# Optimization experiments

Hardware: AMD Instinct MI355X
Metric: run time of the kernel (lower is better)

## Reference

```python
import jax, jax.numpy as jnp
import numpy as np

B, L, HS, WS = 4, 5, 32, 32
C = 256            # dim == heads * dim_head
M, D = 8, 32       # heads, dim_head
T, R = 2, 4        # num_types, num_relations
I = M * D          # inner_dim
EPS = 1e-5


def setup_inputs() -> dict:
    key = jax.random.key(0)
    ks = jax.random.split(key, 12)
    w = 0.02
    x = jax.random.normal(ks[0], (B, L, HS, WS, C), dtype=jnp.float32)
    mask = jnp.ones((B, HS, WS, L, L), dtype=jnp.int32)
    prior_encoding = jax.random.randint(ks[1], (B, L, HS, WS, 3), 0, T).astype(jnp.float32)
    return {
        "x": x,
        "mask": mask,
        "prior_encoding": prior_encoding,
        "ln_w": jnp.ones((C,), jnp.float32),
        "ln_b": jnp.zeros((C,), jnp.float32),
        "Wq": jax.random.normal(ks[2], (T, C, I), jnp.float32) * w,
        "bq": jnp.zeros((T, I), jnp.float32),
        "Wk": jax.random.normal(ks[3], (T, C, I), jnp.float32) * w,
        "bk": jnp.zeros((T, I), jnp.float32),
        "Wv": jax.random.normal(ks[4], (T, C, I), jnp.float32) * w,
        "bv": jnp.zeros((T, I), jnp.float32),
        "Wa": jax.random.normal(ks[5], (T, I, C), jnp.float32) * w,
        "ba": jnp.zeros((T, C), jnp.float32),
        "rel_att": jax.random.normal(ks[6], (R, M, D, D), jnp.float32) * w,
        "rel_msg": jax.random.normal(ks[7], (R, M, D, D), jnp.float32) * w,
    }


def _hgt_forward(x, mask, prior_encoding, ln_w, ln_b, Wq, bq, Wk, bk, Wv, bv, Wa, ba, rel_att, rel_msg):
    # pre-LayerNorm over channel dim
    mu = jnp.mean(x, axis=-1, keepdims=True)
    var = jnp.mean(jnp.square(x - mu), axis=-1, keepdims=True)
    xn = (x - mu) * jax.lax.rsqrt(var + EPS) * ln_w + ln_b

    # [B,L,H,W,C] -> [B,H,W,L,C]
    xp = jnp.transpose(xn, (0, 2, 3, 1, 4))
    types = prior_encoding[:, :, 0, 0, 2].astype(jnp.int32)  # [B,L]

    # per-type q/k/v projections via gather of type-indexed weights
    q = jnp.einsum('bhwlc,blci->bhwli', xp, Wq[types]) + bq[types][:, None, None]
    k = jnp.einsum('bhwlc,blci->bhwli', xp, Wk[types]) + bk[types][:, None, None]
    v = jnp.einsum('bhwlc,blci->bhwli', xp, Wv[types]) + bv[types][:, None, None]

    def to_heads(t):  # [B,H,W,L,I] -> [B,M,H,W,L,D]
        return jnp.transpose(t.reshape(B, HS, WS, L, M, D), (0, 4, 1, 2, 3, 5))
    q, k, v = to_heads(q), to_heads(k), to_heads(v)

    # relation-indexed edge weights: e_type = t_i * T + t_j
    e = types[:, :, None] * T + types[:, None, :]              # [B,L,L]
    w_att = jnp.transpose(rel_att[e], (0, 3, 1, 2, 4, 5))      # [B,M,L,L,D,D]
    w_msg = jnp.transpose(rel_msg[e], (0, 3, 1, 2, 4, 5))

    scale = D ** -0.5
    q_w = jnp.einsum('bmhwip,bmijpq->bmhwijq', q, w_att)
    att = jnp.einsum('bmhwijq,bmhwjq->bmhwij', q_w, k) * scale
    att = jnp.where(mask[:, None] == 0, -1e9, att)
    att = jax.nn.softmax(att, axis=-1)

    v_msg = jnp.einsum('bmijpc,bmhwjp->bmhwijc', w_msg, v)
    out = jnp.einsum('bmhwij,bmhwijc->bmhwic', att, v_msg)

    # [B,M,H,W,L,D] -> [B,H,W,L,C]
    out = jnp.transpose(out, (0, 2, 3, 4, 1, 5)).reshape(B, HS, WS, L, I)
    out = jnp.einsum('bhwli,blic->bhwlc', out, Wa[types]) + ba[types][:, None, None]
    # dropout is identity at inference
    return jnp.transpose(out, (0, 3, 1, 2, 4))                 # [B,L,H,W,C]


def reference(x, mask, prior_encoding, ln_w, ln_b, Wq, bq, Wk, bk, Wv, bv, Wa, ba, rel_att, rel_msg):
    return _hgt_forward(x, mask, prior_encoding, ln_w, ln_b, Wq, bq, Wk, bk, Wv, bv, Wa, ba, rel_att, rel_msg)
```

## Files before the change

### kernel.cpp

```cpp
#include <hip/hip_runtime.h>
#include <hip/hip_bf16.h>
#include <math.h>

#define BB 4
#define LL 5
#define HSZ 32
#define WSZ 32
#define PP (HSZ*WSZ)
#define CC 256
#define MM 8
#define DD 32
#define II 256
#define TT 2
#define NTOK (BB*PP*LL*II)
#define TILE_ELEMS 8192
#define SCALE 0.17677669529663687f

typedef short bf16x8 __attribute__((ext_vector_type(8)));
typedef float f32x4 __attribute__((ext_vector_type(4)));

static __device__ __forceinline__ ushort f2bf(float f) {
    unsigned u = __float_as_uint(f);
    unsigned r = (u + 0x7fffu + ((u >> 16) & 1u)) >> 16;
    return (ushort)r;
}
static __device__ __forceinline__ float bf2f(ushort u) {
    return __uint_as_float(((unsigned)u) << 16);
}

__global__ __launch_bounds__(256) void k_fold(
    const float* __restrict__ Wq, const float* __restrict__ Wv,
    const float* __restrict__ Wk, const float* __restrict__ Wa,
    const float* __restrict__ bq, const float* __restrict__ bv,
    const float* __restrict__ rel_att, const float* __restrict__ rel_msg,
    const float* __restrict__ x,
    const float* __restrict__ lnw, const float* __restrict__ lnb,
    ushort* __restrict__ packW, float* __restrict__ bEff,
    ushort* __restrict__ xnPack)
{
    __shared__ float As[1024];
    __shared__ ushort Apack[8192];
    const int blk = blockIdx.x;
    const int tid = threadIdx.x;

    if (blk < 64) {
        const int p  = blk >> 5;
        const int t  = (blk >> 4) & 1;
        const int ts = (blk >> 3) & 1;
        const int m  = blk & 7;
        const float* A = (p == 0)
            ? rel_att + (size_t)((t * 2 + ts) * 8 + m) * 1024
            : rel_msg + (size_t)((ts * 2 + t) * 8 + m) * 1024;
        for (int i = tid; i < 1024; i += 256) As[i] = A[i];
        __syncthreads();

        const float* W = ((p == 0) ? Wq : Wv) + (size_t)t * 65536;
        const int k = tid;
        float wrow[32];
        #pragma unroll
        for (int u = 0; u < 8; ++u)
            *(float4*)&wrow[u * 4] = *(const float4*)&W[k * 256 + m * 32 + u * 4];

        const int slot = (p == 0 ? 0 : 4) + t * 2 + ts;
        ushort* base = packW + (size_t)slot * 65536;
        const int kt = k >> 5, j = k & 7, lq = ((k >> 3) & 3) * 16;
        #pragma unroll
        for (int q = 0; q < 32; ++q) {
            float acc = 0.f;
            #pragma unroll
            for (int pp = 0; pp < 32; ++pp) acc += wrow[pp] * As[pp * 32 + q];
            const int nt = m * 2 + (q >> 4);
            const int lane = lq + (q & 15);
            base[(size_t)((nt * 8 + kt) * 64 + lane) * 8 + j] = f2bf(acc);
        }
        if (tid < 32) {
            const int q = tid;
            const float* bi = ((p == 0) ? bq : bv) + t * 256 + m * 32;
            float acc = 0.f;
            #pragma unroll
            for (int pp = 0; pp < 32; ++pp) acc += bi[pp] * As[pp * 32 + q];
            bEff[(p ? 1024 : 0) + (t * 2 + ts) * 256 + m * 32 + q] = acc;
        }
    } else if (blk < 192) {
        const int idx = blk - 64;
        const int which = idx >> 6;
        const int gi = (idx & 63) * 256 + tid;
        const int t = gi >> 13;
        const int sub = gi & 8191;
        const float* src = ((which == 0) ? Wk : Wa) + (size_t)t * 65536;
        const int slot = (which == 0 ? 8 : 10) + t;
        const int nt = sub >> 9, kt = (sub >> 6) & 7, lane = sub & 63;
        const int k0 = kt * 32 + (lane >> 4) * 8;
        const int n  = nt * 16 + (lane & 15);
        ushort h[8];
        #pragma unroll
        for (int j = 0; j < 8; ++j) h[j] = f2bf(src[(size_t)(k0 + j) * 256 + n]);
        uint4 o;
        o.x = (unsigned)h[0] | ((unsigned)h[1] << 16);
        o.y = (unsigned)h[2] | ((unsigned)h[3] << 16);
        o.z = (unsigned)h[4] | ((unsigned)h[5] << 16);
        o.w = (unsigned)h[6] | ((unsigned)h[7] << 16);
        *(uint4*)(packW + (size_t)slot * 65536 + (size_t)sub * 8) = o;
    } else {
        const int lblk = blk - 192;
        const int bl  = lblk >> 5;
        const int pt  = lblk & 31;
        const int p0  = pt * 32;

        const int r  = tid >> 3;
        const int jj = tid & 7;
        const float* xrow = x + ((size_t)bl * PP + p0 + r) * CC;
        float4 xv[8];
        float s1 = 0.f, s2 = 0.f;
        #pragma unroll
        for (int u = 0; u < 8; ++u) {
            xv[u] = *(const float4*)(xrow + jj * 32 + u * 4);
            s1 += xv[u].x + xv[u].y + xv[u].z + xv[u].w;
            s2 += xv[u].x * xv[u].x + xv[u].y * xv[u].y + xv[u].z * xv[u].z + xv[u].w * xv[u].w;
        }
        s1 += __shfl_xor(s1, 1); s1 += __shfl_xor(s1, 2); s1 += __shfl_xor(s1, 4);
        s2 += __shfl_xor(s2, 1); s2 += __shfl_xor(s2, 2); s2 += __shfl_xor(s2, 4);
        const float mu   = s1 * (1.0f / 256.0f);
        const float var  = s2 * (1.0f / 256.0f) - mu * mu;
        const float rstd = rsqrtf(var + 1e-5f);

        const int mt_r = r >> 4, rm = r & 15;
        #pragma unroll
        for (int u = 0; u < 8; ++u) {
            const int c0 = jj * 32 + u * 4;
            const float4 g  = *(const float4*)(lnw + c0);
            const float4 bt = *(const float4*)(lnb + c0);
            const ushort h0 = f2bf((xv[u].x - mu) * rstd * g.x + bt.x);
            const ushort h1 = f2bf((xv[u].y - mu) * rstd * g.y + bt.y);
            const ushort h2 = f2bf((xv[u].z - mu) * rstd * g.z + bt.z);
            const ushort h3 = f2bf((xv[u].w - mu) * rstd * g.w + bt.w);
            uint2 w2;
            w2.x = (unsigned)h0 | ((unsigned)h1 << 16);
            w2.y = (unsigned)h2 | ((unsigned)h3 << 16);
            const int kt   = c0 >> 5;
            const int lsub = rm + (((c0 >> 3) & 3) << 4);
            const int j0   = c0 & 7;
            *(uint2*)&Apack[(((mt_r * 8 + kt) * 64 + lsub) << 3) + j0] = w2;
        }
        __syncthreads();

        const size_t tbase = (size_t)lblk * TILE_ELEMS;
        #pragma unroll
        for (int u = 0; u < 4; ++u) {
            const int ch = (tid + u * 256) * 8;
            *(uint4*)&xnPack[tbase + ch] = *(const uint4*)&Apack[ch];
        }
    }
}

__global__ __launch_bounds__(256) void k_proj(
    const ushort* __restrict__ xnPack, const float* __restrict__ prior,
    const ushort* __restrict__ packW, const float* __restrict__ bEff,
    const float* __restrict__ bk,
    ushort* __restrict__ qw0, ushort* __restrict__ qw1, ushort* __restrict__ kkO,
    ushort* __restrict__ vm0, ushort* __restrict__ vm1)
{
    __shared__ ushort As[8192];

    const int tid  = threadIdx.x;
    const int blk  = blockIdx.x;
    const int mat  = blk / 640;
    const int rem  = blk - mat * 640;
    const int bl   = rem >> 5;
    const int sub  = rem & 31;
    const int pg   = sub >> 1;
    const int half = sub & 1;
    const int t    = (int)prior[(size_t)bl * (PP * 3) + 2];

    int slot; const float* bias;
    if (mat < 2)       { slot = t * 2 + mat;           bias = bEff + slot * 256; }
    else if (mat == 2) { slot = 8 + t;                 bias = bk + t * 256; }
    else               { slot = 4 + t * 2 + (mat - 3); bias = bEff + 1024 + (t * 2 + (mat - 3)) * 256; }
    ushort* dst = (mat == 0) ? qw0 : (mat == 1) ? qw1 : (mat == 2) ? kkO : (mat == 3) ? vm0 : vm1;

    const int wv = tid >> 6, lane = tid & 63;

    const ushort* Bp = packW + (size_t)slot * 65536;
    bf16x8 bfr[8][2];
    #pragma unroll
    for (int kt = 0; kt < 8; ++kt)
        #pragma unroll
        for (int nn = 0; nn < 2; ++nn) {
            const int ntg = half * 8 + wv * 2 + nn;
            bfr[kt][nn] = *(const bf16x8*)&Bp[(size_t)((ntg * 8 + kt) * 64 + lane) * 8];
        }

    const int cl = lane & 15, rq = lane >> 4;
    const int colA = half * 128 + wv * 32 + cl;
    const int colB = colA + 16;
    const float biasA = bias[colA], biasB = bias[colB];

    #pragma unroll 1
    for (int tl = 0; tl < 2; ++tl) {
        const int pt = pg * 2 + tl;
        const size_t tbase = (size_t)(bl * 32 + pt) * TILE_ELEMS;
        __syncthreads();
        #pragma unroll
        for (int u = 0; u < 4; ++u) {
            const int ch = (tid + u * 256) * 8;
            *(uint4*)&As[ch] = *(const uint4*)&xnPack[tbase + ch];
        }
        __syncthreads();

        f32x4 acc[2][2];
        #pragma unroll
        for (int mt = 0; mt < 2; ++mt)
            #pragma unroll
            for (int nn = 0; nn < 2; ++nn)
                acc[mt][nn] = (f32x4){0.f, 0.f, 0.f, 0.f};

        #pragma unroll
        for (int kt = 0; kt < 8; ++kt) {
            const bf16x8 a0 = *(const bf16x8*)&As[((0 * 8 + kt) * 64 + lane) << 3];
            const bf16x8 a1 = *(const bf16x8*)&As[((1 * 8 + kt) * 64 + lane) << 3];
            acc[0][0] = __builtin_amdgcn_mfma_f32_16x16x32_bf16(a0, bfr[kt][0], acc[0][0], 0, 0, 0);
            acc[0][1] = __builtin_amdgcn_mfma_f32_16x16x32_bf16(a0, bfr[kt][1], acc[0][1], 0, 0, 0);
            acc[1][0] = __builtin_amdgcn_mfma_f32_16x16x32_bf16(a1, bfr[kt][0], acc[1][0], 0, 0, 0);
            acc[1][1] = __builtin_amdgcn_mfma_f32_16x16x32_bf16(a1, bfr[kt][1], acc[1][1], 0, 0, 0);
        }

        const int p0 = pt * 32;
        #pragma unroll
        for (int mt = 0; mt < 2; ++mt) {
            const int row0 = p0 + mt * 16 + rq * 4;
            #pragma unroll
            for (int r2 = 0; r2 < 4; ++r2) {
                const size_t rb = ((size_t)bl * PP + row0 + r2) * II;
                dst[rb + colA] = f2bf(acc[mt][0][r2] + biasA);
                dst[rb + colB] = f2bf(acc[mt][1][r2] + biasB);
            }
        }
    }
}

__global__ __launch_bounds__(256) void k_attn(
    const ushort* __restrict__ qw0, const ushort* __restrict__ qw1,
    const ushort* __restrict__ kkI,
    const ushort* __restrict__ vm0, const ushort* __restrict__ vm1,
    const int* __restrict__ mask, const float* __restrict__ prior,
    ushort* __restrict__ ao)
{
    const int tid  = threadIdx.x;
    const int site = blockIdx.x * 4 + (tid >> 6);
    const int lane = tid & 63;
    const int b    = site >> 10;
    const int pix  = site & 1023;
    const int c0   = lane * 4;

    const int usite = __builtin_amdgcn_readfirstlane(site);
    const int ub    = usite >> 10;

    int ty[5];
    #pragma unroll
    for (int l = 0; l < 5; ++l)
        ty[l] = (int)prior[(size_t)(ub * 5 + l) * (PP * 3) + 2];

    int mv[5][5];
    #pragma unroll
    for (int i = 0; i < 5; ++i)
        #pragma unroll
        for (int j = 0; j < 5; ++j)
            mv[i][j] = mask[(size_t)usite * 25 + i * 5 + j];

    float qf[2][5][4], kf[5][4];
    #pragma unroll
    for (int l = 0; l < 5; ++l) {
        const size_t base = (((size_t)(b * 5 + l) << 10) + pix) * II + c0;
        const ushort4 q0 = *(const ushort4*)(qw0 + base);
        const ushort4 q1 = *(const ushort4*)(qw1 + base);
        const ushort4 kv = *(const ushort4*)(kkI + base);
        qf[0][l][0] = bf2f(q0.x); qf[0][l][1] = bf2f(q0.y); qf[0][l][2] = bf2f(q0.z); qf[0][l][3] = bf2f(q0.w);
        qf[1][l][0] = bf2f(q1.x); qf[1][l][1] = bf2f(q1.y); qf[1][l][2] = bf2f(q1.z); qf[1][l][3] = bf2f(q1.w);
        kf[l][0]    = bf2f(kv.x); kf[l][1]    = bf2f(kv.y); kf[l][2]    = bf2f(kv.z); kf[l][3]    = bf2f(kv.w);
    }

    float s[5][5];
    #pragma unroll
    for (int j = 0; j < 5; ++j) {
        if (ty[j]) {
            #pragma unroll
            for (int i = 0; i < 5; ++i)
                s[i][j] = qf[1][i][0] * kf[j][0] + qf[1][i][1] * kf[j][1]
                        + qf[1][i][2] * kf[j][2] + qf[1][i][3] * kf[j][3];
        } else {
            #pragma unroll
            for (int i = 0; i < 5; ++i)
                s[i][j] = qf[0][i][0] * kf[j][0] + qf[0][i][1] * kf[j][1]
                        + qf[0][i][2] * kf[j][2] + qf[0][i][3] * kf[j][3];
        }
    }
    #pragma unroll
    for (int i = 0; i < 5; ++i)
        #pragma unroll
        for (int j = 0; j < 5; ++j) s[i][j] += __shfl_xor(s[i][j], 1);
    #pragma unroll
    for (int i = 0; i < 5; ++i)
        #pragma unroll
        for (int j = 0; j < 5; ++j) s[i][j] += __shfl_xor(s[i][j], 2);
    #pragma unroll
    for (int i = 0; i < 5; ++i)
        #pragma unroll
        for (int j = 0; j < 5; ++j) s[i][j] += __shfl_xor(s[i][j], 4);

    float vf[2][5][4];
    #pragma unroll
    for (int l = 0; l < 5; ++l) {
        const size_t base = (((size_t)(b * 5 + l) << 10) + pix) * II + c0;
        const ushort4 v0 = *(const ushort4*)(vm0 + base);
        const ushort4 v1 = *(const ushort4*)(vm1 + base);
        vf[0][l][0] = bf2f(v0.x); vf[0][l][1] = bf2f(v0.y); vf[0][l][2] = bf2f(v0.z); vf[0][l][3] = bf2f(v0.w);
        vf[1][l][0] = bf2f(v1.x); vf[1][l][1] = bf2f(v1.y); vf[1][l][2] = bf2f(v1.z); vf[1][l][3] = bf2f(v1.w);
    }

    #pragma unroll
    for (int i = 0; i < 5; ++i) {
        float lg[5];
        #pragma unroll
        for (int j = 0; j < 5; ++j)
            lg[j] = mv[i][j] ? s[i][j] * SCALE : -1e9f;
        const float mx = fmaxf(fmaxf(fmaxf(lg[0], lg[1]), fmaxf(lg[2], lg[3])), lg[4]);
        float ex[5], sum = 0.f;
        #pragma unroll
        for (int j = 0; j < 5; ++j) { ex[j] = __expf(lg[j] - mx); sum += ex[j]; }
        const float rs = 1.0f / sum;
        float o0 = 0.f, o1 = 0.f, o2 = 0.f, o3 = 0.f;
        if (ty[i]) {
            #pragma unroll
            for (int j = 0; j < 5; ++j) {
                o0 += ex[j] * vf[1][j][0]; o1 += ex[j] * vf[1][j][1];
                o2 += ex[j] * vf[1][j][2]; o3 += ex[j] * vf[1][j][3];
            }
        } else {
            #pragma unroll
            for (int j = 0; j < 5; ++j) {
                o0 += ex[j] * vf[0][j][0]; o1 += ex[j] * vf[0][j][1];
                o2 += ex[j] * vf[0][j][2]; o3 += ex[j] * vf[0][j][3];
            }
        }
        o0 *= rs; o1 *= rs; o2 *= rs; o3 *= rs;
        uint2 w2;
        w2.x = (unsigned)f2bf(o0) | ((unsigned)f2bf(o1) << 16);
        w2.y = (unsigned)f2bf(o2) | ((unsigned)f2bf(o3) << 16);
        *(uint2*)&ao[(((size_t)(b * 5 + i) << 10) + pix) * II + c0] = w2;
    }
}

__global__ __launch_bounds__(256) void k_out(
    const ushort* __restrict__ ao, const float* __restrict__ prior,
    const ushort* __restrict__ packW, const float* __restrict__ ba,
    float* __restrict__ out)
{
    __shared__ float obufF[32 * 132];

    const int tid  = threadIdx.x;
    const int blk  = blockIdx.x;
    const int bl   = blk >> 6;
    const int sub  = blk & 63;
    const int pt   = sub >> 1;
    const int half = sub & 1;
    const int bbi  = bl / LL;
    const int l    = bl - bbi * LL;
    const int t    = (int)prior[(size_t)bl * (PP * 3) + 2];

    const int wv = tid >> 6, lane = tid & 63;
    const ushort* Bp = packW + (size_t)(10 + t) * 65536;
    bf16x8 bfr[8][2];
    #pragma unroll
    for (int kt = 0; kt < 8; ++kt)
        #pragma unroll
        for (int nn = 0; nn < 2; ++nn) {
            const int ntg = half * 8 + wv * 2 + nn;
            bfr[kt][nn] = *(const bf16x8*)&Bp[(size_t)((ntg * 8 + kt) * 64 + lane) * 8];
        }

    const int p0   = pt * 32;
    const int rowA = lane & 15;
    const int ksub = (lane >> 4) * 8;
    const ushort* a_base = ao + ((size_t)(bl * PP + p0 + rowA)) * II + ksub;

    const int cl = lane & 15, rq = lane >> 4;
    const int colL_A = wv * 32 + cl;
    const int colL_B = colL_A + 16;
    const float biasA = ba[t * CC + half * 128 + colL_A];
    const float biasB = ba[t * CC + half * 128 + colL_B];

    f32x4 acc[2][2];
    #pragma unroll
    for (int mt = 0; mt < 2; ++mt)
        #pragma unroll
        for (int nn = 0; nn < 2; ++nn)
            acc[mt][nn] = (f32x4){0.f, 0.f, 0.f, 0.f};

    #pragma unroll
    for (int kt = 0; kt < 8; ++kt) {
        const bf16x8 a0 = *(const bf16x8*)(a_base + kt * 32);
        const bf16x8 a1 = *(const bf16x8*)(a_base + (size_t)16 * II + kt * 32);
        acc[0][0] = __builtin_amdgcn_mfma_f32_16x16x32_bf16(a0, bfr[kt][0], acc[0][0], 0, 0, 0);
        acc[0][1] = __builtin_amdgcn_mfma_f32_16x16x32_bf16(a0, bfr[kt][1], acc[0][1], 0, 0, 0);
        acc[1][0] = __builtin_amdgcn_mfma_f32_16x16x32_bf16(a1, bfr[kt][0], acc[1][0], 0, 0, 0);
        acc[1][1] = __builtin_amdgcn_mfma_f32_16x16x32_bf16(a1, bfr[kt][1], acc[1][1], 0, 0, 0);
    }

    #pragma unroll
    for (int mt = 0; mt < 2; ++mt) {
        const int rowb = mt * 16 + rq * 4;
        #pragma unroll
        for (int r2 = 0; r2 < 4; ++r2) {
            obufF[(rowb + r2) * 132 + colL_A] = acc[mt][0][r2] + biasA;
            obufF[(rowb + r2) * 132 + colL_B] = acc[mt][1][r2] + biasB;
        }
    }
    __syncthreads();

    #pragma unroll
    for (int k2 = 0; k2 < 4; ++k2) {
        const int id  = tid + k2 * 256;
        const int row = id >> 5;
        const int ch  = (id & 31) * 4;
        const float4 v4 = *(const float4*)&obufF[row * 132 + ch];
        *(float4*)(out + ((size_t)(bbi * LL + l) * PP + p0 + row) * CC + half * 128 + ch) = v4;
    }
}

extern "C" void kernel_launch(void* const* d_in, const int* in_sizes, int n_in,
                              void* d_out, int out_size, void* d_ws, size_t ws_size,
                              hipStream_t stream) {
    const float* x       = (const float*)d_in[0];
    const int*   mask    = (const int*)d_in[1];
    const float* prior   = (const float*)d_in[2];
    const float* lnw     = (const float*)d_in[3];
    const float* lnb     = (const float*)d_in[4];
    const float* Wq      = (const float*)d_in[5];
    const float* bq      = (const float*)d_in[6];
    const float* Wk      = (const float*)d_in[7];
    const float* bk      = (const float*)d_in[8];
    const float* Wv      = (const float*)d_in[9];
    const float* bv      = (const float*)d_in[10];
    const float* Wa      = (const float*)d_in[11];
    const float* ba      = (const float*)d_in[12];
    const float* rel_att = (const float*)d_in[13];
    const float* rel_msg = (const float*)d_in[14];
    float* out = (float*)d_out;

    ushort* qw0    = (ushort*)d_ws;
    ushort* qw1    = qw0 + NTOK;
    ushort* kko    = qw1 + NTOK;
    ushort* vm0    = kko + NTOK;
    ushort* vm1    = vm0 + NTOK;
    ushort* ao     = vm1 + NTOK;
    ushort* xnPack = ao + NTOK;
    ushort* packW  = xnPack + NTOK;
    float*  bEff   = (float*)(packW + 12 * 65536);

    hipLaunchKernelGGL(k_fold, dim3(832), dim3(256), 0, stream,
                       Wq, Wv, Wk, Wa, bq, bv, rel_att, rel_msg,
                       x, lnw, lnb, packW, bEff, xnPack);
    hipLaunchKernelGGL(k_proj, dim3(3200), dim3(256), 0, stream,
                       xnPack, prior, packW, bEff, bk, qw0, qw1, kko, vm0, vm1);
    hipLaunchKernelGGL(k_attn, dim3(1024), dim3(256), 0, stream,
                       qw0, qw1, kko, vm0, vm1, mask, prior, ao);
    hipLaunchKernelGGL(k_out, dim3(1280), dim3(256), 0, stream,
                       ao, prior, packW, ba, out);
}
```

Baseline: 154.9 us.

## Fuse four stage kernels into one persistent cooperative kernel with grid syncs

Replaces the four separate launches (fold/LayerNorm, projection, attention, output projection) with one cooperative persistent kernel. Blocks grid-stride over the work of each stage, and grid.sync separates the stages. The projection stage now processes one tile per work unit and reloads the B fragments each time, where before each block handled two tiles. This removes the gaps between launches and the launch overhead. In exchange it adds grid-wide barriers, caps occupancy through launch bounds, and makes every stage share one register and LDS budget.

```diff
diff --git a/kernel.cpp b/kernel.cpp
--- a/kernel.cpp
+++ b/kernel.cpp
@@ -1,6 +1,9 @@
 #include <hip/hip_runtime.h>
+#include <hip/hip_cooperative_groups.h>
 #include <hip/hip_bf16.h>
 #include <math.h>
+
+namespace cg = cooperative_groups;
 
 #define BB 4
 #define LL 5
@@ -28,183 +31,180 @@
     return __uint_as_float(((unsigned)u) << 16);
 }
 
-__global__ __launch_bounds__(256) void k_fold(
-    const float* __restrict__ Wq, const float* __restrict__ Wv,
-    const float* __restrict__ Wk, const float* __restrict__ Wa,
-    const float* __restrict__ bq, const float* __restrict__ bv,
-    const float* __restrict__ rel_att, const float* __restrict__ rel_msg,
-    const float* __restrict__ x,
-    const float* __restrict__ lnw, const float* __restrict__ lnb,
-    ushort* __restrict__ packW, float* __restrict__ bEff,
-    ushort* __restrict__ xnPack)
+struct MegaArgs {
+    const float* x; const int* mask; const float* prior;
+    const float* lnw; const float* lnb;
+    const float* Wq; const float* bq; const float* Wk; const float* bk;
+    const float* Wv; const float* bv; const float* Wa; const float* ba;
+    const float* rel_att; const float* rel_msg;
+    ushort* qw0; ushort* qw1; ushort* kko; ushort* vm0; ushort* vm1;
+    ushort* ao; ushort* xnPack; ushort* packW; float* bEff;
+    float* out;
+};
+
+union SMem {
+    struct { float As[1024]; ushort Apack[8192]; } f;
+    ushort As16[8192];
+    float  obufF[32 * 132];
+};
+
+__global__ __launch_bounds__(256, 4) void k_mega(MegaArgs g)
 {
-    __shared__ float As[1024];
-    __shared__ ushort Apack[8192];
-    const int blk = blockIdx.x;
+    __shared__ SMem sm;
+    cg::grid_group grid = cg::this_grid();
+
     const int tid = threadIdx.x;
-
-    if (blk < 64) {
-        const int p  = blk >> 5;
-        const int t  = (blk >> 4) & 1;
-        const int ts = (blk >> 3) & 1;
-        const int m  = blk & 7;
-        const float* A = (p == 0)
-            ? rel_att + (size_t)((t * 2 + ts) * 8 + m) * 1024
-            : rel_msg + (size_t)((ts * 2 + t) * 8 + m) * 1024;
-        for (int i = tid; i < 1024; i += 256) As[i] = A[i];
+    const int bid = blockIdx.x;
+    const int NB  = gridDim.x;
+    const int wv = tid >> 6, lane = tid & 63;
+
+    for (int blk = bid; blk < 832; blk += NB) {
         __syncthreads();
-
-        const float* W = ((p == 0) ? Wq : Wv) + (size_t)t * 65536;
-        const int k = tid;
-        float wrow[32];
-        #pragma unroll
-        for (int u = 0; u < 8; ++u)
-            *(float4*)&wrow[u * 4] = *(const float4*)&W[k * 256 + m * 32 + u * 4];
-
-        const int slot = (p == 0 ? 0 : 4) + t * 2 + ts;
-        ushort* base = packW + (size_t)slot * 65536;
-        const int kt = k >> 5, j = k & 7, lq = ((k >> 3) & 3) * 16;
-        #pragma unroll
-        for (int q = 0; q < 32; ++q) {
-            float acc = 0.f;
-            #pragma unroll
-            for (int pp = 0; pp < 32; ++pp) acc += wrow[pp] * As[pp * 32 + q];
-            const int nt = m * 2 + (q >> 4);
-            const int lane = lq + (q & 15);
-            base[(size_t)((nt * 8 + kt) * 64 + lane) * 8 + j] = f2bf(acc);
-        }
-        if (tid < 32) {
-            const int q = tid;
-            const float* bi = ((p == 0) ? bq : bv) + t * 256 + m * 32;
-            float acc = 0.f;
-            #pragma unroll
-            for (int pp = 0; pp < 32; ++pp) acc += bi[pp] * As[pp * 32 + q];
-            bEff[(p ? 1024 : 0) + (t * 2 + ts) * 256 + m * 32 + q] = acc;
-        }
-    } else if (blk < 192) {
-        const int idx = blk - 64;
-        const int which = idx >> 6;
-        const int gi = (idx & 63) * 256 + tid;
-        const int t = gi >> 13;
-        const int sub = gi & 8191;
-        const float* src = ((which == 0) ? Wk : Wa) + (size_t)t * 65536;
-        const int slot = (which == 0 ? 8 : 10) + t;
-        const int nt = sub >> 9, kt = (sub >> 6) & 7, lane = sub & 63;
-        const int k0 = kt * 32 + (lane >> 4) * 8;
-        const int n  = nt * 16 + (lane & 15);
-        ushort h[8];
-        #pragma unroll
-        for (int j = 0; j < 8; ++j) h[j] = f2bf(src[(size_t)(k0 + j) * 256 + n]);
-        uint4 o;
-        o.x = (unsigned)h[0] | ((unsigned)h[1] << 16);
-        o.y = (unsigned)h[2] | ((unsigned)h[3] << 16);
-        o.z = (unsigned)h[4] | ((unsigned)h[5] << 16);
-        o.w = (unsigned)h[6] | ((unsigned)h[7] << 16);
-        *(uint4*)(packW + (size_t)slot * 65536 + (size_t)sub * 8) = o;
-    } else {
-        const int lblk = blk - 192;
-        const int bl  = lblk >> 5;
-        const int pt  = lblk & 31;
-        const int p0  = pt * 32;
-
-        const int r  = tid >> 3;
-        const int jj = tid & 7;
-        const float* xrow = x + ((size_t)bl * PP + p0 + r) * CC;
-        float4 xv[8];
-        float s1 = 0.f, s2 = 0.f;
-        #pragma unroll
-        for (int u = 0; u < 8; ++u) {
-            xv[u] = *(const float4*)(xrow + jj * 32 + u * 4);
-            s1 += xv[u].x + xv[u].y + xv[u].z + xv[u].w;
-            s2 += xv[u].x * xv[u].x + xv[u].y * xv[u].y + xv[u].z * xv[u].z + xv[u].w * xv[u].w;
-        }
-        s1 += __shfl_xor(s1, 1); s1 += __shfl_xor(s1, 2); s1 += __shfl_xor(s1, 4);
-        s2 += __shfl_xor(s2, 1); s2 += __shfl_xor(s2, 2); s2 += __shfl_xor(s2, 4);
-        const float mu   = s1 * (1.0f / 256.0f);
-        const float var  = s2 * (1.0f / 256.0f) - mu * mu;
-        const float rstd = rsqrtf(var + 1e-5f);
-
-        const int mt_r = r >> 4, rm = r & 15;
-        #pragma unroll
-        for (int u = 0; u < 8; ++u) {
-            const int c0 = jj * 32 + u * 4;
-            const float4 g  = *(const float4*)(lnw + c0);
-            const float4 bt = *(const float4*)(lnb + c0);
-            const ushort h0 = f2bf((xv[u].x - mu) * rstd * g.x + bt.x);
-            const ushort h1 = f2bf((xv[u].y - mu) * rstd * g.y + bt.y);
-            const ushort h2 = f2bf((xv[u].z - mu) * rstd * g.z + bt.z);
-            const ushort h3 = f2bf((xv[u].w - mu) * rstd * g.w + bt.w);
-            uint2 w2;
-            w2.x = (unsigned)h0 | ((unsigned)h1 << 16);
-            w2.y = (unsigned)h2 | ((unsigned)h3 << 16);
-            const int kt   = c0 >> 5;
-            const int lsub = rm + (((c0 >> 3) & 3) << 4);
-            const int j0   = c0 & 7;
-            *(uint2*)&Apack[(((mt_r * 8 + kt) * 64 + lsub) << 3) + j0] = w2;
-        }
+        if (blk < 64) {
+            const int p  = blk >> 5;
+            const int t  = (blk >> 4) & 1;
+            const int ts = (blk >> 3) & 1;
+            const int m  = blk & 7;
+            const float* A = (p == 0)
+                ? g.rel_att + (size_t)((t * 2 + ts) * 8 + m) * 1024
+                : g.rel_msg + (size_t)((ts * 2 + t) * 8 + m) * 1024;
+            for (int i = tid; i < 1024; i += 256) sm.f.As[i] = A[i];
+            __syncthreads();
+
+            const float* W = ((p == 0) ? g.Wq : g.Wv) + (size_t)t * 65536;
+            const int k = tid;
+            float wrow[32];
+            #pragma unroll
+            for (int u = 0; u < 8; ++u)
+                *(float4*)&wrow[u * 4] = *(const float4*)&W[k * 256 + m * 32 + u * 4];
+
+            const int slot = (p == 0 ? 0 : 4) + t * 2 + ts;
+            ushort* base = g.packW + (size_t)slot * 65536;
+            const int kt = k >> 5, j = k & 7, lq = ((k >> 3) & 3) * 16;
+            #pragma unroll
+            for (int q = 0; q < 32; ++q) {
+                float acc = 0.f;
+                #pragma unroll
+                for (int pp = 0; pp < 32; ++pp) acc += wrow[pp] * sm.f.As[pp * 32 + q];
+                const int nt = m * 2 + (q >> 4);
+                const int ln2 = lq + (q & 15);
+                base[(size_t)((nt * 8 + kt) * 64 + ln2) * 8 + j] = f2bf(acc);
+            }
+            if (tid < 32) {
+                const int q = tid;
+                const float* bi = ((p == 0) ? g.bq : g.bv) + t * 256 + m * 32;
+                float acc = 0.f;
+                #pragma unroll
+                for (int pp = 0; pp < 32; ++pp) acc += bi[pp] * sm.f.As[pp * 32 + q];
+                g.bEff[(p ? 1024 : 0) + (t * 2 + ts) * 256 + m * 32 + q] = acc;
+            }
+        } else if (blk < 192) {
+            const int idx = blk - 64;
+            const int which = idx >> 6;
+            const int gi = (idx & 63) * 256 + tid;
+            const int t = gi >> 13;
+            const int sub = gi & 8191;
+            const float* src = ((which == 0) ? g.Wk : g.Wa) + (size_t)t * 65536;
+            const int slot = (which == 0 ? 8 : 10) + t;
+            const int nt = sub >> 9, kt = (sub >> 6) & 7, ln2 = sub & 63;
+            const int k0 = kt * 32 + (ln2 >> 4) * 8;
+            const int n  = nt * 16 + (ln2 & 15);
+            ushort h[8];
+            #pragma unroll
+            for (int j = 0; j < 8; ++j) h[j] = f2bf(src[(size_t)(k0 + j) * 256 + n]);
+            uint4 o;
+            o.x = (unsigned)h[0] | ((unsigned)h[1] << 16);
+            o.y = (unsigned)h[2] | ((unsigned)h[3] << 16);
+            o.z = (unsigned)h[4] | ((unsigned)h[5] << 16);
+            o.w = (unsigned)h[6] | ((unsigned)h[7] << 16);
+            *(uint4*)(g.packW + (size_t)slot * 65536 + (size_t)sub * 8) = o;
+        } else {
+            const int lblk = blk - 192;
+            const int bl  = lblk >> 5;
+            const int pt  = lblk & 31;
+            const int p0  = pt * 32;
+
+            const int r  = tid >> 3;
+            const int jj = tid & 7;
+            const float* xrow = g.x + ((size_t)bl * PP + p0 + r) * CC;
+            float4 xv[8];
+            float s1 = 0.f, s2 = 0.f;
+            #pragma unroll
+            for (int u = 0; u < 8; ++u) {
+                xv[u] = *(const float4*)(xrow + jj * 32 + u * 4);
+                s1 += xv[u].x + xv[u].y + xv[u].z + xv[u].w;
+                s2 += xv[u].x * xv[u].x + xv[u].y * xv[u].y + xv[u].z * xv[u].z + xv[u].w * xv[u].w;
+            }
+            s1 += __shfl_xor(s1, 1); s1 += __shfl_xor(s1, 2); s1 += __shfl_xor(s1, 4);
+            s2 += __shfl_xor(s2, 1); s2 += __shfl_xor(s2, 2); s2 += __shfl_xor(s2, 4);
+            const float mu   = s1 * (1.0f / 256.0f);
+            const float var  = s2 * (1.0f / 256.0f) - mu * mu;
+            const float rstd = rsqrtf(var + 1e-5f);
+
+            const int mt_r = r >> 4, rm = r & 15;
+            #pragma unroll
+            for (int u = 0; u < 8; ++u) {
+                const int c0 = jj * 32 + u * 4;
+                const float4 gg = *(const float4*)(g.lnw + c0);
+                const float4 bt = *(const float4*)(g.lnb + c0);
+                const ushort h0 = f2bf((xv[u].x - mu) * rstd * gg.x + bt.x);
+                const ushort h1 = f2bf((xv[u].y - mu) * rstd * gg.y + bt.y);
+                const ushort h2 = f2bf((xv[u].z - mu) * rstd * gg.z + bt.z);
+                const ushort h3 = f2bf((xv[u].w - mu) * rstd * gg.w + bt.w);
+                uint2 w2;
+                w2.x = (unsigned)h0 | ((unsigned)h1 << 16);
+                w2.y = (unsigned)h2 | ((unsigned)h3 << 16);
+                const int kt   = c0 >> 5;
+                const int lsub = rm + (((c0 >> 3) & 3) << 4);
+                const int j0   = c0 & 7;
+                *(uint2*)&sm.f.Apack[(((mt_r * 8 + kt) * 64 + lsub) << 3) + j0] = w2;
+            }
+            __syncthreads();
+
+            const size_t tbase = (size_t)lblk * TILE_ELEMS;
+            #pragma unroll
+            for (int u = 0; u < 4; ++u) {
+                const int ch = (tid + u * 256) * 8;
+                *(uint4*)&g.xnPack[tbase + ch] = *(const uint4*)&sm.f.Apack[ch];
+            }
+        }
+    }
+
+    __threadfence();
+    grid.sync();
+
+    for (int u = bid; u < 6400; u += NB) {
+        const int mat  = u / 1280;
+        const int rem  = u - mat * 1280;
+        const int bl   = rem >> 6;
+        const int sub  = rem & 63;
+        const int pt   = sub >> 1;
+        const int half = sub & 1;
+        const int t    = (int)g.prior[(size_t)bl * (PP * 3) + 2];
+
+        int slot; const float* bias;
+        if (mat < 2)       { slot = t * 2 + mat;           bias = g.bEff + slot * 256; }
+        else if (mat == 2) { slot = 8 + t;                 bias = g.bk + t * 256; }
+        else               { slot = 4 + t * 2 + (mat - 3); bias = g.bEff + 1024 + (t * 2 + (mat - 3)) * 256; }
+        ushort* dst = (mat == 0) ? g.qw0 : (mat == 1) ? g.qw1 : (mat == 2) ? g.kko : (mat == 3) ? g.vm0 : g.vm1;
+
         __syncthreads();
-
-        const size_t tbase = (size_t)lblk * TILE_ELEMS;
-        #pragma unroll
-        for (int u = 0; u < 4; ++u) {
-            const int ch = (tid + u * 256) * 8;
-            *(uint4*)&xnPack[tbase + ch] = *(const uint4*)&Apack[ch];
-        }
-    }
-}
-
-__global__ __launch_bounds__(256) void k_proj(
-    const ushort* __restrict__ xnPack, const float* __restrict__ prior,
-    const ushort* __restrict__ packW, const float* __restrict__ bEff,
-    const float* __restrict__ bk,
-    ushort* __restrict__ qw0, ushort* __restrict__ qw1, ushort* __restrict__ kkO,
-    ushort* __restrict__ vm0, ushort* __restrict__ vm1)
-{
-    __shared__ ushort As[8192];
-
-    const int tid  = threadIdx.x;
-    const int blk  = blockIdx.x;
-    const int mat  = blk / 640;
-    const int rem  = blk - mat * 640;
-    const int bl   = rem >> 5;
-    const int sub  = rem & 31;
-    const int pg   = sub >> 1;
-    const int half = sub & 1;
-    const int t    = (int)prior[(size_t)bl * (PP * 3) + 2];
-
-    int slot; const float* bias;
-    if (mat < 2)       { slot = t * 2 + mat;           bias = bEff + slot * 256; }
-    else if (mat == 2) { slot = 8 + t;                 bias = bk + t * 256; }
-    else               { slot = 4 + t * 2 + (mat - 3); bias = bEff + 1024 + (t * 2 + (mat - 3)) * 256; }
-    ushort* dst = (mat == 0) ? qw0 : (mat == 1) ? qw1 : (mat == 2) ? kkO : (mat == 3) ? vm0 : vm1;
-
-    const int wv = tid >> 6, lane = tid & 63;
-
-    const ushort* Bp = packW + (size_t)slot * 65536;
-    bf16x8 bfr[8][2];
-    #pragma unroll
-    for (int kt = 0; kt < 8; ++kt)
-        #pragma unroll
-        for (int nn = 0; nn < 2; ++nn) {
-            const int ntg = half * 8 + wv * 2 + nn;
-            bfr[kt][nn] = *(const bf16x8*)&Bp[(size_t)((ntg * 8 + kt) * 64 + lane) * 8];
-        }
-
-    const int cl = lane & 15, rq = lane >> 4;
-    const int colA = half * 128 + wv * 32 + cl;
-    const int colB = colA + 16;
-    const float biasA = bias[colA], biasB = bias[colB];
-
-    #pragma unroll 1
-    for (int tl = 0; tl < 2; ++tl) {
-        const int pt = pg * 2 + tl;
         const size_t tbase = (size_t)(bl * 32 + pt) * TILE_ELEMS;
-        __syncthreads();
-        #pragma unroll
-        for (int u = 0; u < 4; ++u) {
-            const int ch = (tid + u * 256) * 8;
-            *(uint4*)&As[ch] = *(const uint4*)&xnPack[tbase + ch];
-        }
+        #pragma unroll
+        for (int uu = 0; uu < 4; ++uu) {
+            const int ch = (tid + uu * 256) * 8;
+            *(uint4*)&sm.As16[ch] = *(const uint4*)&g.xnPack[tbase + ch];
+        }
+
+        const ushort* Bp = g.packW + (size_t)slot * 65536;
+        bf16x8 bfr[8][2];
+        #pragma unroll
+        for (int kt = 0; kt < 8; ++kt)
+            #pragma unroll
+            for (int nn = 0; nn < 2; ++nn) {
+                const int ntg = half * 8 + wv * 2 + nn;
+                bfr[kt][nn] = *(const bf16x8*)&Bp[(size_t)((ntg * 8 + kt) * 64 + lane) * 8];
+            }
         __syncthreads();
 
         f32x4 acc[2][2];
@@ -216,14 +216,18 @@
 
         #pragma unroll
         for (int kt = 0; kt < 8; ++kt) {
-            const bf16x8 a0 = *(const bf16x8*)&As[((0 * 8 + kt) * 64 + lane) << 3];
-            const bf16x8 a1 = *(const bf16x8*)&As[((1 * 8 + kt) * 64 + lane) << 3];
+            const bf16x8 a0 = *(const bf16x8*)&sm.As16[((0 * 8 + kt) * 64 + lane) << 3];
+            const bf16x8 a1 = *(const bf16x8*)&sm.As16[((1 * 8 + kt) * 64 + lane) << 3];
             acc[0][0] = __builtin_amdgcn_mfma_f32_16x16x32_bf16(a0, bfr[kt][0], acc[0][0], 0, 0, 0);
             acc[0][1] = __builtin_amdgcn_mfma_f32_16x16x32_bf16(a0, bfr[kt][1], acc[0][1], 0, 0, 0);
             acc[1][0] = __builtin_amdgcn_mfma_f32_16x16x32_bf16(a1, bfr[kt][0], acc[1][0], 0, 0, 0);
             acc[1][1] = __builtin_amdgcn_mfma_f32_16x16x32_bf16(a1, bfr[kt][1], acc[1][1], 0, 0, 0);
         }
 
+        const int cl = lane & 15, rq = lane >> 4;
+        const int colA = half * 128 + wv * 32 + cl;
+        const int colB = colA + 16;
+        const float biasA = bias[colA], biasB = bias[colB];
         const int p0 = pt * 32;
         #pragma unroll
         for (int mt = 0; mt < 2; ++mt) {
@@ -236,234 +240,230 @@
             }
         }
     }
-}
-
-__global__ __launch_bounds__(256) void k_attn(
-    const ushort* __restrict__ qw0, const ushort* __restrict__ qw1,
-    const ushort* __restrict__ kkI,
-    const ushort* __restrict__ vm0, const ushort* __restrict__ vm1,
-    const int* __restrict__ mask, const float* __restrict__ prior,
-    ushort* __restrict__ ao)
-{
-    const int tid  = threadIdx.x;
-    const int site = blockIdx.x * 4 + (tid >> 6);
-    const int lane = tid & 63;
-    const int b    = site >> 10;
-    const int pix  = site & 1023;
-    const int c0   = lane * 4;
-
-    const int usite = __builtin_amdgcn_readfirstlane(site);
-    const int ub    = usite >> 10;
-
-    int ty[5];
-    #pragma unroll
-    for (int l = 0; l < 5; ++l)
-        ty[l] = (int)prior[(size_t)(ub * 5 + l) * (PP * 3) + 2];
-
-    int mv[5][5];
-    #pragma unroll
-    for (int i = 0; i < 5; ++i)
-        #pragma unroll
-        for (int j = 0; j < 5; ++j)
-            mv[i][j] = mask[(size_t)usite * 25 + i * 5 + j];
-
-    float qf[2][5][4], kf[5][4];
-    #pragma unroll
-    for (int l = 0; l < 5; ++l) {
-        const size_t base = (((size_t)(b * 5 + l) << 10) + pix) * II + c0;
-        const ushort4 q0 = *(const ushort4*)(qw0 + base);
-        const ushort4 q1 = *(const ushort4*)(qw1 + base);
-        const ushort4 kv = *(const ushort4*)(kkI + base);
-        qf[0][l][0] = bf2f(q0.x); qf[0][l][1] = bf2f(q0.y); qf[0][l][2] = bf2f(q0.z); qf[0][l][3] = bf2f(q0.w);
-        qf[1][l][0] = bf2f(q1.x); qf[1][l][1] = bf2f(q1.y); qf[1][l][2] = bf2f(q1.z); qf[1][l][3] = bf2f(q1.w);
-        kf[l][0]    = bf2f(kv.x); kf[l][1]    = bf2f(kv.y); kf[l][2]    = bf2f(kv.z); kf[l][3]    = bf2f(kv.w);
+
+    __threadfence();
+    grid.sync();
+
+    for (int u = bid; u < 1024; u += NB) {
+        const int site = u * 4 + (tid >> 6);
+        const int b    = site >> 10;
+        const int pix  = site & 1023;
+        const int c0   = lane * 4;
+
+        const int usite = __builtin_amdgcn_readfirstlane(site);
+        const int ub    = usite >> 10;
+
+        int ty[5];
+        #pragma unroll
+        for (int l = 0; l < 5; ++l)
+            ty[l] = (int)g.prior[(size_t)(ub * 5 + l) * (PP * 3) + 2];
+
+        int mv[5][5];
+        #pragma unroll
+        for (int i = 0; i < 5; ++i)
+            #pragma unroll
+            for (int j = 0; j < 5; ++j)
+                mv[i][j] = g.mask[(size_t)usite * 25 + i * 5 + j];
+
+        float qf[2][5][4], kf[5][4];
+        #pragma unroll
+        for (int l = 0; l < 5; ++l) {
+            const size_t base = (((size_t)(b * 5 + l) << 10) + pix) * II + c0;
+            const ushort4 q0 = *(const ushort4*)(g.qw0 + base);
+            const ushort4 q1 = *(const ushort4*)(g.qw1 + base);
+            const ushort4 kv = *(const ushort4*)(g.kko + base);
+            qf[0][l][0] = bf2f(q0.x); qf[0][l][1] = bf2f(q0.y); qf[0][l][2] = bf2f(q0.z); qf[0][l][3] = bf2f(q0.w);
+            qf[1][l][0] = bf2f(q1.x); qf[1][l][1] = bf2f(q1.y); qf[1][l][2] = bf2f(q1.z); qf[1][l][3] = bf2f(q1.w);
+            kf[l][0]    = bf2f(kv.x); kf[l][1]    = bf2f(kv.y); kf[l][2]    = bf2f(kv.z); kf[l][3]    = bf2f(kv.w);
+        }
+
+        float s[5][5];
+        #pragma unroll
+        for (int j = 0; j < 5; ++j) {
+            if (ty[j]) {
+                #pragma unroll
+                for (int i = 0; i < 5; ++i)
+                    s[i][j] = qf[1][i][0] * kf[j][0] + qf[1][i][1] * kf[j][1]
+                            + qf[1][i][2] * kf[j][2] + qf[1][i][3] * kf[j][3];
+            } else {
+                #pragma unroll
+                for (int i = 0; i < 5; ++i)
+                    s[i][j] = qf[0][i][0] * kf[j][0] + qf[0][i][1] * kf[j][1]
+                            + qf[0][i][2] * kf[j][2] + qf[0][i][3] * kf[j][3];
+            }
+        }
+        #pragma unroll
+        for (int i = 0; i < 5; ++i)
+            #pragma unroll
+            for (int j = 0; j < 5; ++j) s[i][j] += __shfl_xor(s[i][j], 1);
+        #pragma unroll
+        for (int i = 0; i < 5; ++i)
+            #pragma unroll
+            for (int j = 0; j < 5; ++j) s[i][j] += __shfl_xor(s[i][j], 2);
+        #pragma unroll
+        for (int i = 0; i < 5; ++i)
+            #pragma unroll
+            for (int j = 0; j < 5; ++j) s[i][j] += __shfl_xor(s[i][j], 4);
+
+        float vf[2][5][4];
+        #pragma unroll
+        for (int l = 0; l < 5; ++l) {
+            const size_t base = (((size_t)(b * 5 + l) << 10) + pix) * II + c0;
+            const ushort4 v0 = *(const ushort4*)(g.vm0 + base);
+            const ushort4 v1 = *(const ushort4*)(g.vm1 + base);
+            vf[0][l][0] = bf2f(v0.x); vf[0][l][1] = bf2f(v0.y); vf[0][l][2] = bf2f(v0.z); vf[0][l][3] = bf2f(v0.w);
+            vf[1][l][0] = bf2f(v1.x); vf[1][l][1] = bf2f(v1.y); vf[1][l][2] = bf2f(v1.z); vf[1][l][3] = bf2f(v1.w);
+        }
+
+        #pragma unroll
+        for (int i = 0; i < 5; ++i) {
+            float lg[5];
+            #pragma unroll
+            for (int j = 0; j < 5; ++j)
+                lg[j] = mv[i][j] ? s[i][j] * SCALE : -1e9f;
+            const float mx = fmaxf(fmaxf(fmaxf(lg[0], lg[1]), fmaxf(lg[2], lg[3])), lg[4]);
+            float ex[5], sum = 0.f;
+            #pragma unroll
+            for (int j = 0; j < 5; ++j) { ex[j] = __expf(lg[j] - mx); sum += ex[j]; }
+            const float rs = 1.0f / sum;
+            float o0 = 0.f, o1 = 0.f, o2 = 0.f, o3 = 0.f;
+            if (ty[i]) {
+                #pragma unroll
+                for (int j = 0; j < 5; ++j) {
+                    o0 += ex[j] * vf[1][j][0]; o1 += ex[j] * vf[1][j][1];
+                    o2 += ex[j] * vf[1][j][2]; o3 += ex[j] * vf[1][j][3];
+                }
+            } else {
+                #pragma unroll
+                for (int j = 0; j < 5; ++j) {
+                    o0 += ex[j] * vf[0][j][0]; o1 += ex[j] * vf[0][j][1];
+                    o2 += ex[j] * vf[0][j][2]; o3 += ex[j] * vf[0][j][3];
+                }
+            }
+            o0 *= rs; o1 *= rs; o2 *= rs; o3 *= rs;
+            uint2 w2;
+            w2.x = (unsigned)f2bf(o0) | ((unsigned)f2bf(o1) << 16);
+            w2.y = (unsigned)f2bf(o2) | ((unsigned)f2bf(o3) << 16);
+            *(uint2*)&g.ao[(((size_t)(b * 5 + i) << 10) + pix) * II + c0] = w2;
+        }
     }
 
-    float s[5][5];
-    #pragma unroll
-    for (int j = 0; j < 5; ++j) {
-        if (ty[j]) {
-            #pragma unroll
-            for (int i = 0; i < 5; ++i)
-                s[i][j] = qf[1][i][0] * kf[j][0] + qf[1][i][1] * kf[j][1]
-                        + qf[1][i][2] * kf[j][2] + qf[1][i][3] * kf[j][3];
-        } else {
-            #pragma unroll
-            for (int i = 0; i < 5; ++i)
-                s[i][j] = qf[0][i][0] * kf[j][0] + qf[0][i][1] * kf[j][1]
-                        + qf[0][i][2] * kf[j][2] + qf[0][i][3] * kf[j][3];
-        }
-    }
-    #pragma unroll
-    for (int i = 0; i < 5; ++i)
-        #pragma unroll
-        for (int j = 0; j < 5; ++j) s[i][j] += __shfl_xor(s[i][j], 1);
-    #pragma unroll
-    for (int i = 0; i < 5; ++i)
-        #pragma unroll
-        for (int j = 0; j < 5; ++j) s[i][j] += __shfl_xor(s[i][j], 2);
-    #pragma unroll
-    for (int i = 0; i < 5; ++i)
-        #pragma unroll
-        for (int j = 0; j < 5; ++j) s[i][j] += __shfl_xor(s[i][j], 4);
-
-    float vf[2][5][4];
-    #pragma unroll
-    for (int l = 0; l < 5; ++l) {
-        const size_t base = (((size_t)(b * 5 + l) << 10) + pix) * II + c0;
-        const ushort4 v0 = *(const ushort4*)(vm0 + base);
-        const ushort4 v1 = *(const ushort4*)(vm1 + base);
-        vf[0][l][0] = bf2f(v0.x); vf[0][l][1] = bf2f(v0.y); vf[0][l][2] = bf2f(v0.z); vf[0][l][3] = bf2f(v0.w);
-        vf[1][l][0] = bf2f(v1.x); vf[1][l][1] = bf2f(v1.y); vf[1][l][2] = bf2f(v1.z); vf[1][l][3] = bf2f(v1.w);
-    }
-
-    #pragma unroll
-    for (int i = 0; i < 5; ++i) {
-        float lg[5];
-        #pragma unroll
-        for (int j = 0; j < 5; ++j)
-            lg[j] = mv[i][j] ? s[i][j] * SCALE : -1e9f;
-        const float mx = fmaxf(fmaxf(fmaxf(lg[0], lg[1]), fmaxf(lg[2], lg[3])), lg[4]);
-        float ex[5], sum = 0.f;
-        #pragma unroll
-        for (int j = 0; j < 5; ++j) { ex[j] = __expf(lg[j] - mx); sum += ex[j]; }
-        const float rs = 1.0f / sum;
-        float o0 = 0.f, o1 = 0.f, o2 = 0.f, o3 = 0.f;
-        if (ty[i]) {
-            #pragma unroll
-            for (int j = 0; j < 5; ++j) {
-                o0 += ex[j] * vf[1][j][0]; o1 += ex[j] * vf[1][j][1];
-                o2 += ex[j] * vf[1][j][2]; o3 += ex[j] * vf[1][j][3];
-            }
-        } else {
-            #pragma unroll
-            for (int j = 0; j < 5; ++j) {
-                o0 += ex[j] * vf[0][j][0]; o1 += ex[j] * vf[0][j][1];
-                o2 += ex[j] * vf[0][j][2]; o3 += ex[j] * vf[0][j][3];
-            }
-        }
-        o0 *= rs; o1 *= rs; o2 *= rs; o3 *= rs;
-        uint2 w2;
-        w2.x = (unsigned)f2bf(o0) | ((unsigned)f2bf(o1) << 16);
-        w2.y = (unsigned)f2bf(o2) | ((unsigned)f2bf(o3) << 16);
-        *(uint2*)&ao[(((size_t)(b * 5 + i) << 10) + pix) * II + c0] = w2;
-    }
-}
-
-__global__ __launch_bounds__(256) void k_out(
-    const ushort* __restrict__ ao, const float* __restrict__ prior,
-    const ushort* __restrict__ packW, const float* __restrict__ ba,
-    float* __restrict__ out)
-{
-    __shared__ float obufF[32 * 132];
-
-    const int tid  = threadIdx.x;
-    const int blk  = blockIdx.x;
-    const int bl   = blk >> 6;
-    const int sub  = blk & 63;
-    const int pt   = sub >> 1;
-    const int half = sub & 1;
-    const int bbi  = bl / LL;
-    const int l    = bl - bbi * LL;
-    const int t    = (int)prior[(size_t)bl * (PP * 3) + 2];
-
-    const int wv = tid >> 6, lane = tid & 63;
-    const ushort* Bp = packW + (size_t)(10 + t) * 65536;
-    bf16x8 bfr[8][2];
-    #pragma unroll
-    for (int kt = 0; kt < 8; ++kt)
-        #pragma unroll
-        for (int nn = 0; nn < 2; ++nn) {
-            const int ntg = half * 8 + wv * 2 + nn;
-            bfr[kt][nn] = *(const bf16x8*)&Bp[(size_t)((ntg * 8 + kt) * 64 + lane) * 8];
-        }
-
-    const int p0   = pt * 32;
-    const int rowA = lane & 15;
-    const int ksub = (lane >> 4) * 8;
-    const ushort* a_base = ao + ((size_t)(bl * PP + p0 + rowA)) * II + ksub;
-
-    const int cl = lane & 15, rq = lane >> 4;
-    const int colL_A = wv * 32 + cl;
-    const int colL_B = colL_A + 16;
-    const float biasA = ba[t * CC + half * 128 + colL_A];
-    const float biasB = ba[t * CC + half * 128 + colL_B];
-
-    f32x4 acc[2][2];
-    #pragma unroll
-    for (int mt = 0; mt < 2; ++mt)
-        #pragma unroll
-        for (int nn = 0; nn < 2; ++nn)
-            acc[mt][nn] = (f32x4){0.f, 0.f, 0.f, 0.f};
-
-    #pragma unroll
-    for (int kt = 0; kt < 8; ++kt) {
-        const bf16x8 a0 = *(const bf16x8*)(a_base + kt * 32);
-        const bf16x8 a1 = *(const bf16x8*)(a_base + (size_t)16 * II + kt * 32);
-        acc[0][0] = __builtin_amdgcn_mfma_f32_16x16x32_bf16(a0, bfr[kt][0], acc[0][0], 0, 0, 0);
-        acc[0][1] = __builtin_amdgcn_mfma_f32_16x16x32_bf16(a0, bfr[kt][1], acc[0][1], 0, 0, 0);
-        acc[1][0] = __builtin_amdgcn_mfma_f32_16x16x32_bf16(a1, bfr[kt][0], acc[1][0], 0, 0, 0);
-        acc[1][1] = __builtin_amdgcn_mfma_f32_16x16x32_bf16(a1, bfr[kt][1], acc[1][1], 0, 0, 0);
-    }
-
-    #pragma unroll
-    for (int mt = 0; mt < 2; ++mt) {
-        const int rowb = mt * 16 + rq * 4;
-        #pragma unroll
-        for (int r2 = 0; r2 < 4; ++r2) {
-            obufF[(rowb + r2) * 132 + colL_A] = acc[mt][0][r2] + biasA;
-            obufF[(rowb + r2) * 132 + colL_B] = acc[mt][1][r2] + biasB;
-        }
-    }
-    __syncthreads();
-
-    #pragma unroll
-    for (int k2 = 0; k2 < 4; ++k2) {
-        const int id  = tid + k2 * 256;
-        const int row = id >> 5;
-        const int ch  = (id & 31) * 4;
-        const float4 v4 = *(const float4*)&obufF[row * 132 + ch];
-        *(float4*)(out + ((size_t)(bbi * LL + l) * PP + p0 + row) * CC + half * 128 + ch) = v4;
+    __threadfence();
+    grid.sync();
+
+    for (int u = bid; u < 1280; u += NB) {
+        __syncthreads();
+        const int bl   = u >> 6;
+        const int sub  = u & 63;
+        const int pt   = sub >> 1;
+        const int half = sub & 1;
+        const int t    = (int)g.prior[(size_t)bl * (PP * 3) + 2];
+
+        const ushort* Bp = g.packW + (size_t)(10 + t) * 65536;
+        bf16x8 bfr[8][2];
+        #pragma unroll
+        for (int kt = 0; kt < 8; ++kt)
+            #pragma unroll
+            for (int nn = 0; nn < 2; ++nn) {
+                const int ntg = half * 8 + wv * 2 + nn;
+                bfr[kt][nn] = *(const bf16x8*)&Bp[(size_t)((ntg * 8 + kt) * 64 + lane) * 8];
+            }
+
+        const int p0   = pt * 32;
+        const int rowA = lane & 15;
+        const int ksub = (lane >> 4) * 8;
+        const ushort* a_base = g.ao + ((size_t)(bl * PP + p0 + rowA)) * II + ksub;
+
+        const int cl = lane & 15, rq = lane >> 4;
+        const int colL_A = wv * 32 + cl;
+        const int colL_B = colL_A + 16;
+        const float biasA = g.ba[t * CC + half * 128 + colL_A];
+        const float biasB = g.ba[t * CC + half * 128 + colL_B];
+
+        f32x4 acc[2][2];
+        #pragma unroll
+        for (int mt = 0; mt < 2; ++mt)
+            #pragma unroll
+            for (int nn = 0; nn < 2; ++nn)
+                acc[mt][nn] = (f32x4){0.f, 0.f, 0.f, 0.f};
+
+        #pragma unroll
+        for (int kt = 0; kt < 8; ++kt) {
+            const bf16x8 a0 = *(const bf16x8*)(a_base + kt * 32);
+            const bf16x8 a1 = *(const bf16x8*)(a_base + (size_t)16 * II + kt * 32);
+            acc[0][0] = __builtin_amdgcn_mfma_f32_16x16x32_bf16(a0, bfr[kt][0], acc[0][0], 0, 0, 0);
+            acc[0][1] = __builtin_amdgcn_mfma_f32_16x16x32_bf16(a0, bfr[kt][1], acc[0][1], 0, 0, 0);
+            acc[1][0] = __builtin_amdgcn_mfma_f32_16x16x32_bf16(a1, bfr[kt][0], acc[1][0], 0, 0, 0);
+            acc[1][1] = __builtin_amdgcn_mfma_f32_16x16x32_bf16(a1, bfr[kt][1], acc[1][1], 0, 0, 0);
+        }
+
+        #pragma unroll
+        for (int mt = 0; mt < 2; ++mt) {
+            const int rowb = mt * 16 + rq * 4;
+            #pragma unroll
+            for (int r2 = 0; r2 < 4; ++r2) {
+                sm.obufF[(rowb + r2) * 132 + colL_A] = acc[mt][0][r2] + biasA;
+                sm.obufF[(rowb + r2) * 132 + colL_B] = acc[mt][1][r2] + biasB;
+            }
+        }
+        __syncthreads();
+
+        #pragma unroll
+        for (int k2 = 0; k2 < 4; ++k2) {
+            const int id  = tid + k2 * 256;
+            const int row = id >> 5;
+            const int ch  = (id & 31) * 4;
+            const float4 v4 = *(const float4*)&sm.obufF[row * 132 + ch];
+            *(float4*)(g.out + ((size_t)bl * PP + p0 + row) * CC + half * 128 + ch) = v4;
+        }
     }
 }
 
 extern "C" void kernel_launch(void* const* d_in, const int* in_sizes, int n_in,
                               void* d_out, int out_size, void* d_ws, size_t ws_size,
                               hipStream_t stream) {
-    const float* x       = (const float*)d_in[0];
-    const int*   mask    = (const int*)d_in[1];
-    const float* prior   = (const float*)d_in[2];
-    const float* lnw     = (const float*)d_in[3];
-    const float* lnb     = (const float*)d_in[4];
-    const float* Wq      = (const float*)d_in[5];
-    const float* bq      = (const float*)d_in[6];
-    const float* Wk      = (const float*)d_in[7];
-    const float* bk      = (const float*)d_in[8];
-    const float* Wv      = (const float*)d_in[9];
-    const float* bv      = (const float*)d_in[10];
-    const float* Wa      = (const float*)d_in[11];
-    const float* ba      = (const float*)d_in[12];
-    const float* rel_att = (const float*)d_in[13];
-    const float* rel_msg = (const float*)d_in[14];
-    float* out = (float*)d_out;
+    MegaArgs ga;
+    ga.x       = (const float*)d_in[0];
+    ga.mask    = (const int*)d_in[1];
+    ga.prior   = (const float*)d_in[2];
+    ga.lnw     = (const float*)d_in[3];
+    ga.lnb     = (const float*)d_in[4];
+    ga.Wq      = (const float*)d_in[5];
+    ga.bq      = (const float*)d_in[6];
+    ga.Wk      = (const float*)d_in[7];
+    ga.bk      = (const float*)d_in[8];
+    ga.Wv      = (const float*)d_in[9];
+    ga.bv      = (const float*)d_in[10];
+    ga.Wa      = (const float*)d_in[11];
+    ga.ba      = (const float*)d_in[12];
+    ga.rel_att = (const float*)d_in[13];
+    ga.rel_msg = (const float*)d_in[14];
+    ga.out     = (float*)d_out;
 
     ushort* qw0    = (ushort*)d_ws;
-    ushort* qw1    = qw0 + NTOK;
-    ushort* kko    = qw1 + NTOK;
-    ushort* vm0    = kko + NTOK;
-    ushort* vm1    = vm0 + NTOK;
-    ushort* ao     = vm1 + NTOK;
-    ushort* xnPack = ao + NTOK;
-    ushort* packW  = xnPack + NTOK;
-    float*  bEff   = (float*)(packW + 12 * 65536);
-
-    hipLaunchKernelGGL(k_fold, dim3(832), dim3(256), 0, stream,
-                       Wq, Wv, Wk, Wa, bq, bv, rel_att, rel_msg,
-                       x, lnw, lnb, packW, bEff, xnPack);
-    hipLaunchKernelGGL(k_proj, dim3(3200), dim3(256), 0, stream,
-                       xnPack, prior, packW, bEff, bk, qw0, qw1, kko, vm0, vm1);
-    hipLaunchKernelGGL(k_attn, dim3(1024), dim3(256), 0, stream,
-                       qw0, qw1, kko, vm0, vm1, mask, prior, ao);
-    hipLaunchKernelGGL(k_out, dim3(1280), dim3(256), 0, stream,
-                       ao, prior, packW, ba, out);
+    ga.qw0    = qw0;
+    ga.qw1    = qw0 + NTOK;
+    ga.kko    = qw0 + 2 * (size_t)NTOK;
+    ga.vm0    = qw0 + 3 * (size_t)NTOK;
+    ga.vm1    = qw0 + 4 * (size_t)NTOK;
+    ga.ao     = qw0 + 5 * (size_t)NTOK;
+    ga.xnPack = qw0 + 6 * (size_t)NTOK;
+    ga.packW  = qw0 + 7 * (size_t)NTOK;
+    ga.bEff   = (float*)(ga.packW + 12 * 65536);
+
+    static int maxBlocksPerCU = -1;
+    if (maxBlocksPerCU < 0) {
+        int nb = 0;
+        if (hipOccupancyMaxActiveBlocksPerMultiprocessor(
+                &nb, reinterpret_cast<const void*>(k_mega), 256, 0) != hipSuccess || nb < 1)
+            nb = 2;
+        maxBlocksPerCU = nb;
+    }
+    int grid = maxBlocksPerCU * 256;
+    if (grid > 1024) grid = 1024;
+    if (grid < 256)  grid = 256;
+
+    void* args[] = { &ga };
+    hipLaunchCooperativeKernel(reinterpret_cast<void*>(k_mega),
+                               dim3(grid), dim3(256), args, 0, stream);
 }
```

Measured after the change: 546.0 us. +252.4%, slower.
